# Kernel optimization log

Hardware: AMD Instinct MI355X
Metric: run time of the kernel (lower is better)

## Reference

```python
import jax, jax.numpy as jnp
import numpy as np

HID = 256   # hidden_dim
P = 16      # pool_size
EPS = 1e-5


def _ln(x, g, b):
    m = x.mean(-1, keepdims=True)
    v = x.var(-1, keepdims=True)
    return (x - m) * jax.lax.rsqrt(v + EPS) * g + b


def setup_inputs() -> dict:
    key = jax.random.key(0)
    ks = jax.random.split(key, 12)
    B, Cf, H, W = 8, 512, 64, 64
    Cg = Cf // 2
    Co = Cf // 2
    s = 0.02
    d = {}
    d['e_f'] = jax.random.normal(ks[0], (B, Cf, H, W), jnp.float32)
    d['e_g'] = jax.random.normal(ks[1], (B, Cg, H, W), jnp.float32)
    d['l_feat'] = jax.random.normal(ks[2], (B, 768, 20), jnp.float32)
    d['l_mask'] = jnp.ones((B, 20, 1), jnp.float32)
    d['ln_f_g'] = jnp.ones((Cf,), jnp.float32)
    d['ln_f_b'] = jnp.zeros((Cf,), jnp.float32)
    d['ln_g_g'] = jnp.ones((Cg,), jnp.float32)
    d['ln_g_b'] = jnp.zeros((Cg,), jnp.float32)
    d['wq'] = jax.random.normal(ks[3], (Cf, HID), jnp.float32) * s
    d['bq'] = jnp.zeros((HID,), jnp.float32)
    d['wk'] = jax.random.normal(ks[4], (Cg, HID), jnp.float32) * s
    d['bk'] = jnp.zeros((HID,), jnp.float32)
    d['wv'] = jax.random.normal(ks[5], (Cg, HID), jnp.float32) * s
    d['bv'] = jnp.zeros((HID,), jnp.float32)
    d['wo'] = jax.random.normal(ks[6], (HID, HID), jnp.float32) * s
    d['bo'] = jnp.zeros((HID,), jnp.float32)
    d['dw_k'] = jax.random.normal(ks[7], (HID, 1, 3, 3), jnp.float32) * s  # depthwise kernel (OIHW, I=1)
    d['efp_w'] = jax.random.normal(ks[8], (HID, Cf), jnp.float32) * s     # 1x1 conv v_channels->hidden
    d['efp_b'] = jnp.zeros((HID,), jnp.float32)
    d['outc_w'] = jax.random.normal(ks[9], (Co, HID), jnp.float32) * s    # 1x1 conv hidden->out
    d['outc_b'] = jnp.zeros((Co,), jnp.float32)
    d['bn_g'] = jnp.ones((Co,), jnp.float32)
    d['bn_b'] = jnp.zeros((Co,), jnp.float32)
    d['bn_m'] = jnp.zeros((Co,), jnp.float32)
    d['bn_v'] = jnp.ones((Co,), jnp.float32)
    return d


def reference(e_f, e_g, l_feat, l_mask, ln_f_g, ln_f_b, ln_g_g, ln_g_b,
              wq, bq, wk, bk, wv, bv, wo, bo, dw_k, efp_w, efp_b,
              outc_w, outc_b, bn_g, bn_b, bn_m, bn_v):
    B, Cf, H, W = e_f.shape
    # Q = w_qi(LN(e_f))                                  (B, HW, HID)
    q = _ln(e_f.transpose(0, 2, 3, 1), ln_f_g, ln_f_b).reshape(B, H * W, Cf) @ wq + bq
    # K/V projections from LN(e_g)
    g = _ln(e_g.transpose(0, 2, 3, 1), ln_g_g, ln_g_b).reshape(B, H * W, -1)
    k = (g @ wk + bk).reshape(B, H, W, HID)
    v = (g @ wv + bv).reshape(B, H, W, HID)
    # 16x16 max/avg pooling -> (B, Hp*Wp, HID)
    k = jnp.max(k.reshape(B, H // P, P, W // P, P, HID), axis=(2, 4)).reshape(B, -1, HID)
    v = jnp.mean(v.reshape(B, H // P, P, W // P, P, HID), axis=(2, 4)).reshape(B, -1, HID)
    # pooled attention
    attn = jax.nn.softmax(jnp.einsum('bqd,bkd->bqk', q, k) * (HID ** -0.5), axis=-1)
    a_i = jnp.einsum('bqk,bkd->bqd', attn, v)  # (B, HW, HID)
    # depthwise 3x3 conv on Q (NCHW)
    q_nchw = q.reshape(B, H, W, HID).transpose(0, 3, 1, 2)
    dw = jax.lax.conv_general_dilated(q_nchw, dw_k, (1, 1), [(1, 1), (1, 1)],
                                      feature_group_count=HID)
    combined = dw + a_i.reshape(B, H, W, HID).transpose(0, 3, 1, 2)
    comb = combined.transpose(0, 2, 3, 1).reshape(B, H * W, HID) @ wo + bo
    comb = comb.reshape(B, H, W, HID).transpose(0, 3, 1, 2)
    # 1x1 proj of e_f, elementwise gate
    efp = jnp.einsum('bchw,oc->bohw', e_f, efp_w) + efp_b[None, :, None, None]
    e_a = efp * comb
    # out: 1x1 conv + BN (inference) + ReLU (dropout inactive in eval)
    out = jnp.einsum('bchw,oc->bohw', e_a, outc_w) + outc_b[None, :, None, None]
    scale = (bn_g * jax.lax.rsqrt(bn_v + EPS))[None, :, None, None]
    out = (out - bn_m[None, :, None, None]) * scale + bn_b[None, :, None, None]
    return jax.nn.relu(out)
```

## Files before the change

### kernel.cpp

```cpp
#include <hip/hip_runtime.h>
#include <math.h>

#define EPS 1e-5f

typedef __attribute__((ext_vector_type(8))) short bf16x8;
typedef __attribute__((ext_vector_type(4))) float f32x4;

__device__ __forceinline__ unsigned short f2bf(float f) {
    unsigned int u = __float_as_uint(f);
    u += 0x7fff + ((u >> 16) & 1);
    return (unsigned short)(u >> 16);
}
__device__ __forceinline__ float bf2f(unsigned short h) {
    return __uint_as_float(((unsigned int)h) << 16);
}
__device__ __forceinline__ float lof(unsigned int u) {
    return __uint_as_float(u << 16);
}
__device__ __forceinline__ float hif(unsigned int u) {
    return __uint_as_float(u & 0xffff0000u);
}
__device__ __forceinline__ void async16(void* lds, const void* g) {
    __builtin_amdgcn_global_load_lds(
        (const __attribute__((address_space(1))) unsigned int*)g,
        (__attribute__((address_space(3))) unsigned int*)lds, 16, 0, 0);
}

__global__ __launch_bounds__(256) void trans_prep(
    const float* __restrict__ ef, const float* __restrict__ eg,
    unsigned short* __restrict__ ef_bf, unsigned short* __restrict__ eg_bf,
    float* __restrict__ pf, float* __restrict__ pfq,
    float* __restrict__ pg, float* __restrict__ pgq,
    const float* __restrict__ lnfg, const float* __restrict__ lnfb,
    const float* __restrict__ wq, const float* __restrict__ bq,
    const float* __restrict__ efpw, const float* __restrict__ efpb,
    const float* __restrict__ lngg, const float* __restrict__ lngb,
    const float* __restrict__ wk, const float* __restrict__ bk,
    const float* __restrict__ wv, const float* __restrict__ bv,
    const float* __restrict__ wo, const float* __restrict__ outcw,
    const float* __restrict__ outcb, const float* __restrict__ bng,
    const float* __restrict__ bnb, const float* __restrict__ bnm,
    const float* __restrict__ bnv, const float* __restrict__ dwk,
    unsigned short* __restrict__ Wb1t, unsigned short* __restrict__ Wb2t,
    unsigned short* __restrict__ Wot, unsigned short* __restrict__ Woc,
    float* __restrict__ dwt,
    float* __restrict__ cs1, float* __restrict__ cst1,
    float* __restrict__ cs2, float* __restrict__ cst2,
    float* __restrict__ scv, float* __restrict__ shv)
{
    __shared__ float tile[64][65];
    __shared__ float psum[4][64], pss[4][64];
    int id = blockIdx.x;
    int t = threadIdx.x;
    if (id < 3072) {
        const float* src; unsigned short* dst; float* ps; float* pq;
        int C, cblk, b, p0;
        if (id < 2048) {
            src = ef; dst = ef_bf; ps = pf; pq = pfq; C = 512;
            b = id >> 8; cblk = (id >> 5) & 7; p0 = (id & 31) * 128;
        } else {
            id -= 2048;
            src = eg; dst = eg_bf; ps = pg; pq = pgq; C = 256;
            b = id >> 7; cblk = (id >> 5) & 3; p0 = (id & 31) * 128;
        }
        int c0 = cblk * 64;
        const float* s = src + ((size_t)b * C + c0) * 4096 + p0;
        int cr = t >> 4, p4 = (t & 15) * 4;
        int lane = t & 63, grp = t >> 6;
        int pr = t >> 3, c8 = (t & 7) * 8;

        float4 r1[4], r2[4];
#pragma unroll
        for (int i = 0; i < 4; i++)
            r1[i] = *(const float4*)(s + (size_t)(i * 16 + cr) * 4096 + p4);
#pragma unroll
        for (int i = 0; i < 4; i++)
            r2[i] = *(const float4*)(s + (size_t)(i * 16 + cr) * 4096 + 64 + p4);

#pragma unroll
        for (int half = 0; half < 2; half++) {
#pragma unroll
            for (int i = 0; i < 4; i++) {
                float4 v = half ? r2[i] : r1[i];
                int c = i * 16 + cr;
                tile[c][p4 + 0] = v.x; tile[c][p4 + 1] = v.y;
                tile[c][p4 + 2] = v.z; tile[c][p4 + 3] = v.w;
            }
            __syncthreads();

            int pbase = p0 + half * 64;
            unsigned short* d = dst + ((size_t)(b * 4096 + pbase)) * C + c0;
#pragma unroll
            for (int i = 0; i < 2; i++) {
                int p = i * 32 + pr;
                uint4 pk;
                pk.x = (unsigned)f2bf(tile[c8 + 0][p]) | ((unsigned)f2bf(tile[c8 + 1][p]) << 16);
                pk.y = (unsigned)f2bf(tile[c8 + 2][p]) | ((unsigned)f2bf(tile[c8 + 3][p]) << 16);
                pk.z = (unsigned)f2bf(tile[c8 + 4][p]) | ((unsigned)f2bf(tile[c8 + 5][p]) << 16);
                pk.w = (unsigned)f2bf(tile[c8 + 6][p]) | ((unsigned)f2bf(tile[c8 + 7][p]) << 16);
                *(uint4*)(d + (size_t)p * C + c8) = pk;
            }

            float sm = 0.f, sq = 0.f;
#pragma unroll
            for (int j = 0; j < 16; j++) {
                float v = tile[grp * 16 + j][lane];
                sm += v; sq += v * v;
            }
            psum[grp][lane] = sm; pss[grp][lane] = sq;
            __syncthreads();
            if (t < 64) {
                float fs = psum[0][t] + psum[1][t] + psum[2][t] + psum[3][t];
                float fq = pss[0][t] + pss[1][t] + pss[2][t] + pss[3][t];
                ps[cblk * 32768 + b * 4096 + pbase + t] = fs;
                pq[cblk * 32768 + b * 4096 + pbase + t] = fq;
            }
            if (half == 0) __syncthreads();
        }
    } else {
        int id2 = id - 3072;
        float* red1 = (float*)psum;
        float* red2 = (float*)pss;
        if (id2 < 64) {
            const float* src; unsigned short* dst; const float* scale;
            int K, k0, n0;
            if (id2 < 32) {
                src = wq; dst = Wb1t; scale = lnfg; K = 512;
                k0 = (id2 >> 2) * 64; n0 = (id2 & 3) * 64;
            } else if (id2 < 48) {
                int j = id2 - 32;
                src = wk; dst = Wb2t; scale = lngg; K = 256;
                k0 = (j >> 2) * 64; n0 = (j & 3) * 64;
            } else {
                int j = id2 - 48;
                src = wo; dst = Wot; scale = nullptr; K = 256;
                k0 = (j >> 2) * 64; n0 = (j & 3) * 64;
            }
            int rr = t >> 6, cc = t & 63;
#pragma unroll
            for (int i = 0; i < 16; i++) {
                int r = i * 4 + rr;
                tile[r][cc] = src[(size_t)(k0 + r) * 256 + n0 + cc];
            }
            __syncthreads();
            int nn = t >> 3, k8 = (t & 7) * 8;
#pragma unroll
            for (int i = 0; i < 2; i++) {
                int n = i * 32 + nn;
                float v[8];
#pragma unroll
                for (int j = 0; j < 8; j++) {
                    float s = scale ? scale[k0 + k8 + j] : 1.f;
                    v[j] = s * tile[k8 + j][n];
                }
                uint4 pk;
                pk.x = (unsigned)f2bf(v[0]) | ((unsigned)f2bf(v[1]) << 16);
                pk.y = (unsigned)f2bf(v[2]) | ((unsigned)f2bf(v[3]) << 16);
                pk.z = (unsigned)f2bf(v[4]) | ((unsigned)f2bf(v[5]) << 16);
                pk.w = (unsigned)f2bf(v[6]) | ((unsigned)f2bf(v[7]) << 16);
                *(uint4*)(dst + (size_t)(n0 + n) * K + k0 + k8) = pk;
            }
        } else if (id2 < 192) {
            int j = (id2 - 64) * 1024 + t * 4;
            float4 v = *(const float4*)(efpw + j);
            uint2 pk;
            pk.x = (unsigned)f2bf(v.x) | ((unsigned)f2bf(v.y) << 16);
            pk.y = (unsigned)f2bf(v.z) | ((unsigned)f2bf(v.w) << 16);
            *(uint2*)(Wb1t + 131072 + j) = pk;
        } else if (id2 < 256) {
            int j = (id2 - 192) * 1024 + t * 4;
            float4 v = *(const float4*)(outcw + j);
            uint2 pk;
            pk.x = (unsigned)f2bf(v.x) | ((unsigned)f2bf(v.y) << 16);
            pk.y = (unsigned)f2bf(v.z) | ((unsigned)f2bf(v.w) << 16);
            *(uint2*)(Woc + j) = pk;
        } else if (id2 == 256) {
#pragma unroll
            for (int tap = 0; tap < 9; tap++)
                dwt[tap * 256 + t] = dwk[t * 9 + tap];
        } else if (id2 < 265) {
            int n0 = (id2 - 257) * 32;
            int nl = t & 31, kq = t >> 5;
            float cs = 0.f, ct = 0.f;
#pragma unroll 4
            for (int kk = 0; kk < 64; kk++) {
                int k = kq * 64 + kk;
                float w = wq[k * 256 + n0 + nl];
                cs += lnfg[k] * w; ct += lnfb[k] * w;
            }
            red1[kq * 32 + nl] = cs; red2[kq * 32 + nl] = ct;
            __syncthreads();
            if (t < 32) {
                float s = 0.f, c2 = 0.f;
#pragma unroll
                for (int q = 0; q < 8; q++) { s += red1[q * 32 + t]; c2 += red2[q * 32 + t]; }
                int n = n0 + t;
                cs1[n] = s; cst1[n] = c2 + bq[n];
                cs1[256 + n] = 0.f; cst1[256 + n] = efpb[n];
            }
        } else if (id2 < 273) {
            int n0 = (id2 - 265) * 32;
            int nl = t & 31, kq = t >> 5;
            float cs = 0.f, ct = 0.f;
#pragma unroll 4
            for (int kk = 0; kk < 32; kk++) {
                int k = kq * 32 + kk;
                float w = wk[k * 256 + n0 + nl];
                cs += lngg[k] * w; ct += lngb[k] * w;
            }
            red1[kq * 32 + nl] = cs; red2[kq * 32 + nl] = ct;
            __syncthreads();
            if (t < 32) {
                float s = 0.f, c2 = 0.f;
#pragma unroll
                for (int q = 0; q < 8; q++) { s += red1[q * 32 + t]; c2 += red2[q * 32 + t]; }
                int n = n0 + t;
                cs2[n] = s; cst2[n] = c2 + bk[n];
            }
        } else if (id2 < 281) {
            int n0 = (id2 - 273) * 32;
            int nl = t & 31, kq = t >> 5;
            float cs = 0.f, ct = 0.f;
#pragma unroll 4
            for (int kk = 0; kk < 32; kk++) {
                int k = kq * 32 + kk;
                float w = wv[k * 256 + n0 + nl];
                cs += lngg[k] * w; ct += lngb[k] * w;
            }
            red1[kq * 32 + nl] = cs; red2[kq * 32 + nl] = ct;
            __syncthreads();
            if (t < 32) {
                float s = 0.f, c2 = 0.f;
#pragma unroll
                for (int q = 0; q < 8; q++) { s += red1[q * 32 + t]; c2 += red2[q * 32 + t]; }
                int n = n0 + t;
                cs2[256 + n] = s; cst2[256 + n] = c2 + bv[n];
            }
        } else {
            int n = t;
            float s = bng[n] * rsqrtf(bnv[n] + EPS);
            scv[n] = s;
            shv[n] = (outcb[n] - bnm[n]) * s + bnb[n];
        }
    }
}

template<int K>
__device__ __forceinline__ void mfma_core(
    const unsigned short* __restrict__ A, const unsigned short* __restrict__ Bt,
    int m0, int n0, unsigned short* As, unsigned short* Bs, f32x4 acc[4][4])
{
    const int tid = threadIdx.x;
    const int wave = tid >> 6, lane = tid & 63;
    const int wm = (wave & 1) * 64, wn = (wave >> 1) * 64;
#pragma unroll
    for (int i = 0; i < 4; i++)
#pragma unroll
        for (int j = 0; j < 4; j++) acc[i][j] = (f32x4){0.f, 0.f, 0.f, 0.f};

    const int srow = wave * 32 + (lane >> 3);
    const int sg = (lane & 7) ^ ((lane >> 3) & 7);
    const unsigned short* ga = A + (size_t)(m0 + srow) * K + sg * 8;
    const unsigned short* gb = Bt + (size_t)(n0 + srow) * K + sg * 8;

    for (int k0 = 0; k0 < K; k0 += 64) {
#pragma unroll
        for (int t = 0; t < 4; t++) {
            async16(As + (wave * 32 + t * 8) * 64, ga + (size_t)t * 8 * K + k0);
            async16(Bs + (wave * 32 + t * 8) * 64, gb + (size_t)t * 8 * K + k0);
        }
        __syncthreads();
#pragma unroll
        for (int ks = 0; ks < 2; ks++) {
            bf16x8 af[4], bfr[4];
            int kb = ks * 4 + (lane >> 4);
            int slot = (kb ^ (lane & 7)) * 8;
#pragma unroll
            for (int i = 0; i < 4; i++) {
                int m = wm + i * 16 + (lane & 15);
                af[i] = *(const bf16x8*)&As[m * 64 + slot];
                int n = wn + i * 16 + (lane & 15);
                bfr[i] = *(const bf16x8*)&Bs[n * 64 + slot];
            }
#pragma unroll
            for (int i = 0; i < 4; i++)
#pragma unroll
                for (int j = 0; j < 4; j++)
                    acc[i][j] = __builtin_amdgcn_mfma_f32_16x16x32_bf16(
                        af[i], bfr[j], acc[i][j], 0, 0, 0);
        }
        __syncthreads();
    }
}

__global__ __launch_bounds__(256, 2) void gemm_proj(
    const unsigned short* __restrict__ ef_bf, const unsigned short* __restrict__ Wb1t,
    const float* __restrict__ cs1, const float* __restrict__ cst1,
    const float* __restrict__ pf, const float* __restrict__ pfq,
    unsigned short* __restrict__ qbuf, unsigned short* __restrict__ efpbuf,
    const unsigned short* __restrict__ eg_bf, const unsigned short* __restrict__ Wb2t,
    const float* __restrict__ cs2, const float* __restrict__ cst2,
    const float* __restrict__ pg, const float* __restrict__ pgq,
    unsigned short* __restrict__ kfull,
    const float* __restrict__ eg, float* __restrict__ s1,
    float* __restrict__ s0)
{
    __shared__ unsigned short As[128 * 64];
    __shared__ unsigned short Bs[256 * 64];
    __shared__ float sstat[256];
    const int tid = threadIdx.x;
    const int wave = tid >> 6, lane = tid & 63;
    const int bid = blockIdx.x;

    if (bid < 512) {
        float* smem = (float*)Bs;
        const int id3 = bid;
        int b = id3 >> 6, hp = (id3 >> 4) & 3, cgrp = id3 & 15;
        int rr = tid >> 4, cq = tid & 15;
        int p = (hp * 16 + rr) * 64 + cq * 4;

        float w[4], m[4];
#pragma unroll
        for (int d = 0; d < 4; d++) {
            int gp = b * 4096 + p + d;
            float s = 0.f, q = 0.f;
#pragma unroll
            for (int i = 0; i < 4; i++) { s += pg[i * 32768 + gp]; q += pgq[i * 32768 + gp]; }
            float mean = s * (1.f / 256.f);
            m[d] = mean;
            w[d] = rsqrtf(q * (1.f / 256.f) - mean * mean + EPS);
        }

        float part[16];
        const float* egb = eg + ((size_t)b * 256 + cgrp * 16) * 4096 + p;
#pragma unroll
        for (int cc = 0; cc < 16; cc++) {
            float4 v4 = *(const float4*)(egb + (size_t)cc * 4096);
            part[cc] = w[0] * v4.x + w[1] * v4.y + w[2] * v4.z + w[3] * v4.w;
        }
#pragma unroll
        for (int cc = 0; cc < 16; cc++) smem[tid * 16 + cc] = part[cc];
        if (cgrp == 0)
            smem[4096 + tid] = w[0] * m[0] + w[1] * m[1] + w[2] * m[2] + w[3] * m[3];
        __syncthreads();
        if (tid < 64) {
            int cx2 = tid >> 4, cc = tid & 15;
            float sacc = 0.f;
#pragma unroll
            for (int rr2 = 0; rr2 < 16; rr2++)
#pragma unroll
                for (int dq = 0; dq < 4; dq++)
                    sacc += smem[(rr2 * 16 + cx2 * 4 + dq) * 16 + cc];
            s1[((size_t)(b * 16 + hp * 4 + cx2)) * 256 + cgrp * 16 + cc] = sacc;
        }
        if (cgrp == 0 && tid < 4) {
            float sacc = 0.f;
#pragma unroll
            for (int rr2 = 0; rr2 < 16; rr2++)
#pragma unroll
                for (int dq = 0; dq < 4; dq++)
                    sacc += smem[4096 + rr2 * 16 + tid * 4 + dq];
            s0[b * 16 + hp * 4 + tid] = sacc;
        }
    } else if (bid < 1024) {
        const int bid1 = bid - 512;
        const int m0 = (bid1 >> 1) * 128, n0 = (bid1 & 1) * 256;
        const int wm = (wave & 1) * 64, wn = (wave >> 1) * 128;
        f32x4 acc[4][8];

        if (tid < 128) {
            int gm = m0 + tid;
            float s = 0.f, q = 0.f;
#pragma unroll
            for (int i = 0; i < 8; i++) { s += pf[i * 32768 + gm]; q += pfq[i * 32768 + gm]; }
            float m = s * (1.f / 512.f);
            sstat[tid] = m;
            sstat[128 + tid] = rsqrtf(q * (1.f / 512.f) - m * m + EPS);
        }

#pragma unroll
        for (int i = 0; i < 4; i++)
#pragma unroll
            for (int j = 0; j < 8; j++) acc[i][j] = (f32x4){0.f, 0.f, 0.f, 0.f};

        const int srow = lane >> 3;
        const int sg = (lane & 7) ^ (srow & 7);
        const unsigned short* ga = ef_bf + (size_t)(m0 + wave * 32 + srow) * 512 + sg * 8;
        const unsigned short* gb = Wb1t + (size_t)(n0 + wave * 64 + srow) * 512 + sg * 8;

        for (int k0 = 0; k0 < 512; k0 += 64) {
#pragma unroll
            for (int t = 0; t < 4; t++)
                async16(As + (wave * 32 + t * 8) * 64, ga + (size_t)t * 8 * 512 + k0);
#pragma unroll
            for (int t = 0; t < 8; t++)
                async16(Bs + (wave * 64 + t * 8) * 64, gb + (size_t)t * 8 * 512 + k0);
            __syncthreads();
#pragma unroll
            for (int ks = 0; ks < 2; ks++) {
                bf16x8 af[4], bfr[8];
                int kb = ks * 4 + (lane >> 4);
                int slot = (kb ^ (lane & 7)) * 8;
#pragma unroll
                for (int i = 0; i < 4; i++)
                    af[i] = *(const bf16x8*)&As[(wm + i * 16 + (lane & 15)) * 64 + slot];
#pragma unroll
                for (int j = 0; j < 8; j++)
                    bfr[j] = *(const bf16x8*)&Bs[(wn + j * 16 + (lane & 15)) * 64 + slot];
#pragma unroll
                for (int i = 0; i < 4; i++)
#pragma unroll
                    for (int j = 0; j < 8; j++)
                        acc[i][j] = __builtin_amdgcn_mfma_f32_16x16x32_bf16(
                            af[i], bfr[j], acc[i][j], 0, 0, 0);
            }
            __syncthreads();
        }

        bool isq = (n0 == 0);
#pragma unroll
        for (int i = 0; i < 4; i++) {
#pragma unroll
            for (int r = 0; r < 4; r++) {
                int lm = wm + i * 16 + ((lane >> 4) * 4) + r;
                int gm = m0 + lm;
                float mean = sstat[lm], rs = sstat[128 + lm];
#pragma unroll
                for (int j = 0; j < 8; j++) {
                    int nn = wn + j * 16 + (lane & 15);
                    float v = acc[i][j][r];
                    if (isq) {
                        int n = nn;
                        float o = rs * (v - mean * cs1[n]) + cst1[n];
                        qbuf[(size_t)gm * 256 + nn] = f2bf(o);
                    } else {
                        int n = nn + 256;
                        efpbuf[(size_t)gm * 256 + nn] = f2bf(v + cst1[n]);
                    }
                }
            }
        }
    } else {
        const int j2 = bid - 1024;
        const int m0 = (j2 >> 1) * 128, n0 = (j2 & 1) * 128;
        f32x4 acc[4][4];

        if (tid < 128) {
            int gm = m0 + tid;
            float s = 0.f, q = 0.f;
#pragma unroll
            for (int i = 0; i < 4; i++) { s += pg[i * 32768 + gm]; q += pgq[i * 32768 + gm]; }
            float m = s * (1.f / 256.f);
            float r = rsqrtf(q * (1.f / 256.f) - m * m + EPS);
            sstat[tid] = m; sstat[128 + tid] = r;
        }

        mfma_core<256>(eg_bf, Wb2t, m0, n0, As, Bs, acc);
        int wm = (wave & 1) * 64, wn = (wave >> 1) * 64;
#pragma unroll
        for (int i = 0; i < 4; i++) {
#pragma unroll
            for (int r = 0; r < 4; r++) {
                int lm = wm + i * 16 + ((lane >> 4) * 4) + r;
                int gm = m0 + lm;
                float mean = sstat[lm], rs = sstat[128 + lm];
#pragma unroll
                for (int j = 0; j < 4; j++) {
                    int n = n0 + wn + j * 16 + (lane & 15);
                    float o = rs * (acc[i][j][r] - mean * cs2[n]) + cst2[n];
                    kfull[(size_t)gm * 256 + n] = f2bf(o);
                }
            }
        }
    }
}

__global__ __launch_bounds__(256) void pool_vp(
    const unsigned short* __restrict__ kfull, unsigned short* __restrict__ kpb,
    const float* __restrict__ s1, const float* __restrict__ s0,
    const float* __restrict__ lngg, const float* __restrict__ wv,
    const float* __restrict__ cs2, const float* __restrict__ cst2,
    float* __restrict__ vp)
{
    __shared__ float smem[2048];
    int id = blockIdx.x;
    int t = threadIdx.x;
    if (id < 128) {
        int b = id >> 4, cell = id & 15;
        int hp = cell >> 2, wp = cell & 3;
        int g8 = t & 31, rr = t >> 5;
        float kmx[8];
#pragma unroll
        for (int j = 0; j < 8; j++) kmx[j] = -3.402823466e38f;
#pragma unroll
        for (int rsub = 0; rsub < 2; rsub++) {
            int r = rr * 2 + rsub;
            int prow = (hp * 16 + r) * 64 + wp * 16;
            for (int cl = 0; cl < 16; cl++) {
                size_t basei = ((size_t)(b * 4096 + prow + cl)) * 256 + g8 * 8;
                uint4 kv = *(const uint4*)(kfull + basei);
                kmx[0] = fmaxf(kmx[0], lof(kv.x)); kmx[1] = fmaxf(kmx[1], hif(kv.x));
                kmx[2] = fmaxf(kmx[2], lof(kv.y)); kmx[3] = fmaxf(kmx[3], hif(kv.y));
                kmx[4] = fmaxf(kmx[4], lof(kv.z)); kmx[5] = fmaxf(kmx[5], hif(kv.z));
                kmx[6] = fmaxf(kmx[6], lof(kv.w)); kmx[7] = fmaxf(kmx[7], hif(kv.w));
            }
        }
#pragma unroll
        for (int j = 0; j < 8; j++) smem[rr * 256 + g8 * 8 + j] = kmx[j];
        __syncthreads();
        float m = smem[t];
#pragma unroll
        for (int r2 = 1; r2 < 8; r2++) m = fmaxf(m, smem[r2 * 256 + t]);
        kpb[(size_t)(b * 16 + cell) * 256 + t] = f2bf(m);
    } else {
        int cell = id - 128;
        int n = t;
        const float* s1r = s1 + (size_t)cell * 256;
        float acc = 0.f;
        for (int c = 0; c < 256; c++)
            acc = fmaf(lngg[c] * s1r[c], wv[c * 256 + n], acc);
        vp[(size_t)cell * 256 + n] = acc * (1.f / 256.f)
            - (s0[cell] * (1.f / 256.f)) * cs2[256 + n] + cst2[256 + n];
    }
}

__global__ __launch_bounds__(256) void combined_dw(
    const unsigned short* __restrict__ qbuf, const unsigned short* __restrict__ kpb,
    const float* __restrict__ vp, const float* __restrict__ dwt,
    unsigned short* __restrict__ combined)
{
    __shared__ float attns[1024];
    int wave = threadIdx.x >> 6, lane = threadIdx.x & 63;
    int id = blockIdx.x;
    int b = id & 7, row = id >> 3;
    int pidx0 = row * 64 + wave * 16;
    int h = row;

    {
        int fr = lane & 15, quad = lane >> 4;
        const unsigned short* qrow =
            qbuf + (size_t)(b * 4096 + pidx0 + fr) * 256 + quad * 8;
        const unsigned short* krow = kpb + (size_t)(b * 16 + fr) * 256 + quad * 8;
        f32x4 sacc = {0.f, 0.f, 0.f, 0.f};
#pragma unroll
        for (int ks = 0; ks < 8; ks++) {
            bf16x8 af = *(const bf16x8*)(qrow + ks * 32);
            bf16x8 bf_ = *(const bf16x8*)(krow + ks * 32);
            sacc = __builtin_amdgcn_mfma_f32_16x16x32_bf16(af, bf_, sacc, 0, 0, 0);
        }
#pragma unroll
        for (int r = 0; r < 4; r++) {
            float s = sacc[r] * 0.0625f;
            float mx = s;
#pragma unroll
            for (int off = 8; off >= 1; off >>= 1) mx = fmaxf(mx, __shfl_xor(mx, off));
            float e = __expf(s - mx);
            float sum = e;
#pragma unroll
            for (int off = 8; off >= 1; off >>= 1) sum += __shfl_xor(sum, off);
            attns[wave * 256 + (quad * 4 + r) * 16 + fr] = e / sum;
        }
    }
    __syncthreads();

    int o4 = lane * 4;
    float4 kreg[9];
#pragma unroll
    for (int tap = 0; tap < 9; tap++)
        kreg[tap] = *(const float4*)&dwt[tap * 256 + o4];
    const float* arow_base = attns + wave * 256;

#pragma unroll
    for (int sub = 0; sub < 4; sub++) {
        int pidx = pidx0 + sub * 4;
        int w0 = pidx & 63;
        float4 acc[4];
#pragma unroll
        for (int i = 0; i < 4; i++) acc[i] = (float4){0.f, 0.f, 0.f, 0.f};
#pragma unroll
        for (int c = 0; c < 16; c++) {
            float4 v = *(const float4*)&vp[(size_t)(b * 16 + c) * 256 + o4];
#pragma unroll
            for (int i = 0; i < 4; i++) {
                float a = arow_base[(sub * 4 + i) * 16 + c];
                acc[i].x = fmaf(a, v.x, acc[i].x); acc[i].y = fmaf(a, v.y, acc[i].y);
                acc[i].z = fmaf(a, v.z, acc[i].z); acc[i].w = fmaf(a, v.w, acc[i].w);
            }
        }
#pragma unroll
        for (int dy = 0; dy < 3; dy++) {
            int hh = h + dy - 1;
            if (hh < 0 || hh > 63) continue;
            const unsigned short* qr = qbuf + ((size_t)(b * 4096 + hh * 64)) * 256;
            float4 ft[6];
#pragma unroll
            for (int c = 0; c < 6; c++) {
                int xx = w0 - 1 + c;
                if (xx < 0 || xx > 63) {
                    ft[c] = (float4){0.f, 0.f, 0.f, 0.f};
                } else {
                    uint2 qa = *(const uint2*)(qr + (size_t)xx * 256 + o4);
                    ft[c] = (float4){lof(qa.x), hif(qa.x), lof(qa.y), hif(qa.y)};
                }
            }
#pragma unroll
            for (int dx = 0; dx < 3; dx++) {
                float4 kk = kreg[dy * 3 + dx];
#pragma unroll
                for (int i = 0; i < 4; i++) {
                    float4 qv = ft[i + dx];
                    acc[i].x = fmaf(qv.x, kk.x, acc[i].x);
                    acc[i].y = fmaf(qv.y, kk.y, acc[i].y);
                    acc[i].z = fmaf(qv.z, kk.z, acc[i].z);
                    acc[i].w = fmaf(qv.w, kk.w, acc[i].w);
                }
            }
        }
#pragma unroll
        for (int i = 0; i < 4; i++) {
            uint2 pk;
            pk.x = (unsigned)f2bf(acc[i].x) | ((unsigned)f2bf(acc[i].y) << 16);
            pk.y = (unsigned)f2bf(acc[i].z) | ((unsigned)f2bf(acc[i].w) << 16);
            *(uint2*)(combined + ((size_t)(b * 4096 + pidx + i)) * 256 + o4) = pk;
        }
    }
}

__global__ __launch_bounds__(256) void gemm34_mfma(
    const unsigned short* __restrict__ comb, const unsigned short* __restrict__ Wot,
    const float* __restrict__ bo, const unsigned short* __restrict__ efp,
    const unsigned short* __restrict__ Woc,
    const float* __restrict__ scv, const float* __restrict__ shv,
    float* __restrict__ outp)
{
    __shared__ unsigned short As[64 * 64];
    __shared__ unsigned short Bs[256 * 64];
    __shared__ unsigned short eat[64 * 256];
    const int tid = threadIdx.x;
    const int wave = tid >> 6, lane = tid & 63;
    const int m0 = blockIdx.x * 64;

    const int srow = lane >> 3;
    const int sg = (lane & 7) ^ (srow & 7);

    f32x4 acc[4][4];
#pragma unroll
    for (int i = 0; i < 4; i++)
#pragma unroll
        for (int j = 0; j < 4; j++) acc[i][j] = (f32x4){0.f, 0.f, 0.f, 0.f};

    const unsigned short* ga = comb + (size_t)(m0 + wave * 16 + srow) * 256 + sg * 8;
    const unsigned short* gb = Wot + (size_t)(wave * 64 + srow) * 256 + sg * 8;

    for (int k0 = 0; k0 < 256; k0 += 64) {
#pragma unroll
        for (int t = 0; t < 2; t++)
            async16(As + (wave * 16 + t * 8) * 64, ga + (size_t)t * 8 * 256 + k0);
#pragma unroll
        for (int t = 0; t < 8; t++)
            async16(Bs + (wave * 64 + t * 8) * 64, gb + (size_t)t * 8 * 256 + k0);
        __syncthreads();
#pragma unroll
        for (int ks = 0; ks < 2; ks++) {
            bf16x8 af[4], bfr[4];
            int kb = ks * 4 + (lane >> 4);
            int slot = (kb ^ (lane & 7)) * 8;
#pragma unroll
            for (int i = 0; i < 4; i++) {
                af[i]  = *(const bf16x8*)&As[(i * 16 + (lane & 15)) * 64 + slot];
                bfr[i] = *(const bf16x8*)&Bs[(wave * 64 + i * 16 + (lane & 15)) * 64 + slot];
            }
#pragma unroll
            for (int i = 0; i < 4; i++)
#pragma unroll
                for (int j = 0; j < 4; j++)
                    acc[i][j] = __builtin_amdgcn_mfma_f32_16x16x32_bf16(
                        af[i], bfr[j], acc[i][j], 0, 0, 0);
        }
        __syncthreads();
    }

    float bo4[4];
#pragma unroll
    for (int j = 0; j < 4; j++) bo4[j] = bo[wave * 64 + j * 16 + (lane & 15)];
#pragma unroll
    for (int i = 0; i < 4; i++) {
#pragma unroll
        for (int r = 0; r < 4; r++) {
            int pos = i * 16 + ((lane >> 4) * 4) + r;
#pragma unroll
            for (int j = 0; j < 4; j++) {
                int n = wave * 64 + j * 16 + (lane & 15);
                float o = (acc[i][j][r] + bo4[j])
                          * bf2f(efp[(size_t)(m0 + pos) * 256 + n]);
                int o8 = j * 2 + ((lane >> 3) & 1);
                int slot = o8 ^ (pos & 7);
                eat[pos * 256 + wave * 64 + slot * 8 + (lane & 7)] = f2bf(o);
            }
        }
    }

    f32x4 acc2[4][4];
#pragma unroll
    for (int i = 0; i < 4; i++)
#pragma unroll
        for (int j = 0; j < 4; j++) acc2[i][j] = (f32x4){0.f, 0.f, 0.f, 0.f};

    const unsigned short* gw = Woc + (size_t)(wave * 64 + srow) * 256 + sg * 8;
    for (int k0 = 0; k0 < 256; k0 += 64) {
#pragma unroll
        for (int t = 0; t < 8; t++)
            async16(Bs + (wave * 64 + t * 8) * 64, gw + (size_t)t * 8 * 256 + k0);
        __syncthreads();
        int kc = k0 >> 6;
#pragma unroll
        for (int ks = 0; ks < 2; ks++) {
            bf16x8 af2[4], bf2_[4];
            int kb = ks * 4 + (lane >> 4);
            int slot = (kb ^ (lane & 7)) * 8;
#pragma unroll
            for (int i = 0; i < 4; i++) {
                af2[i]  = *(const bf16x8*)&Bs[(wave * 64 + i * 16 + (lane & 15)) * 64 + slot];
                bf2_[i] = *(const bf16x8*)&eat[(i * 16 + (lane & 15)) * 256 + kc * 64 + slot];
            }
#pragma unroll
            for (int i = 0; i < 4; i++)
#pragma unroll
                for (int j = 0; j < 4; j++)
                    acc2[i][j] = __builtin_amdgcn_mfma_f32_16x16x32_bf16(
                        af2[i], bf2_[j], acc2[i][j], 0, 0, 0);
        }
        __syncthreads();
    }

#pragma unroll
    for (int i = 0; i < 4; i++) {
#pragma unroll
        for (int r = 0; r < 4; r++) {
            int co = wave * 64 + i * 16 + ((lane >> 4) * 4) + r;
            float s = scv[co], hh = shv[co];
#pragma unroll
            for (int j = 0; j < 4; j++) {
                int p = m0 + j * 16 + (lane & 15);
                float o = fmaxf(fmaf(acc2[i][j][r], s, hh), 0.f);
                outp[((size_t)(p >> 12)) * 1048576 + (size_t)co * 4096 + (p & 4095)] = o;
            }
        }
    }
}

extern "C" void kernel_launch(void* const* d_in, const int* in_sizes, int n_in,
                              void* d_out, int out_size, void* d_ws, size_t ws_size,
                              hipStream_t stream)
{
    const float* e_f   = (const float*)d_in[0];
    const float* e_g   = (const float*)d_in[1];
    const float* lnfg  = (const float*)d_in[4];
    const float* lnfb  = (const float*)d_in[5];
    const float* lngg  = (const float*)d_in[6];
    const float* lngb  = (const float*)d_in[7];
    const float* wq    = (const float*)d_in[8];
    const float* bq    = (const float*)d_in[9];
    const float* wk    = (const float*)d_in[10];
    const float* bk    = (const float*)d_in[11];
    const float* wv    = (const float*)d_in[12];
    const float* bv    = (const float*)d_in[13];
    const float* wo    = (const float*)d_in[14];
    const float* bo    = (const float*)d_in[15];
    const float* dwk   = (const float*)d_in[16];
    const float* efpw  = (const float*)d_in[17];
    const float* efpb  = (const float*)d_in[18];
    const float* outcw = (const float*)d_in[19];
    const float* outcb = (const float*)d_in[20];
    const float* bng   = (const float*)d_in[21];
    const float* bnb   = (const float*)d_in[22];
    const float* bnm   = (const float*)d_in[23];
    const float* bnv   = (const float*)d_in[24];
    float* outp = (float*)d_out;

    char* base = (char*)d_ws;
    auto alloc = [&](size_t bytes) -> char* {
        char* r = base; base += (bytes + 255) & ~(size_t)255; return r;
    };
    float* pf    = (float*)alloc(8 * 32768 * 4);
    float* pfq   = (float*)alloc(8 * 32768 * 4);
    float* pg    = (float*)alloc(4 * 32768 * 4);
    float* pgq   = (float*)alloc(4 * 32768 * 4);
    float* cs1   = (float*)alloc(512 * 4);
    float* cst1  = (float*)alloc(512 * 4);
    float* cs2   = (float*)alloc(512 * 4);
    float* cst2  = (float*)alloc(512 * 4);
    float* scv   = (float*)alloc(256 * 4);
    float* shv   = (float*)alloc(256 * 4);
    float* dwt   = (float*)alloc(9 * 256 * 4);
    unsigned short* Wb1t = (unsigned short*)alloc(262144 * 2);
    unsigned short* Wb2t = (unsigned short*)alloc(65536 * 2);
    unsigned short* Wot  = (unsigned short*)alloc(65536 * 2);
    unsigned short* Woc  = (unsigned short*)alloc(65536 * 2);
    unsigned short* ef_bf = (unsigned short*)alloc((size_t)32768 * 512 * 2);
    unsigned short* eg_bf = (unsigned short*)alloc((size_t)32768 * 256 * 2);
    unsigned short* qbuf  = (unsigned short*)alloc((size_t)32768 * 256 * 2);
    unsigned short* efpbuf = (unsigned short*)alloc((size_t)32768 * 256 * 2);
    unsigned short* kfull = (unsigned short*)alloc((size_t)32768 * 256 * 2);
    unsigned short* kpb  = (unsigned short*)alloc(128 * 256 * 2);
    float* vp    = (float*)alloc(128 * 256 * 4);
    float* s1    = (float*)alloc(128 * 256 * 4);
    float* s0    = (float*)alloc(128 * 4);

    trans_prep<<<3354, 256, 0, stream>>>(
        e_f, e_g, ef_bf, eg_bf, pf, pfq, pg, pgq,
        lnfg, lnfb, wq, bq, efpw, efpb, lngg, lngb, wk, bk, wv, bv, wo,
        outcw, outcb, bng, bnb, bnm, bnv, dwk,
        Wb1t, Wb2t, Wot, Woc, dwt, cs1, cst1, cs2, cst2, scv, shv);
    gemm_proj<<<1536, 256, 0, stream>>>(
        ef_bf, Wb1t, cs1, cst1, pf, pfq, qbuf, efpbuf,
        eg_bf, Wb2t, cs2, cst2, pg, pgq, kfull,
        e_g, s1, s0);
    pool_vp<<<256, 256, 0, stream>>>(kfull, kpb, s1, s0, lngg, wv, cs2, cst2, vp);
    combined_dw<<<512, 256, 0, stream>>>(qbuf, kpb, vp, dwt, kfull);
    gemm34_mfma<<<512, 256, 0, stream>>>(kfull, Wot, bo, efpbuf,
                                         Woc, scv, shv, outp);
}
```

Before: 287.5 us.

## Double-buffer LDS tiles in projection GEMMs to overlap loads with MFMA

Both GEMM paths in gemm_proj now keep two LDS buffers with a K-step of 32 instead of one buffer with a K-step of 64. The next tile is prefetched asynchronously while MFMAs run on the current one, leaving one barrier per step instead of two. The LDS swizzle is rewritten for the narrower 32-wide rows. The aim is to hide global-load latency behind compute, at the cost of twice as many loop iterations and a changed bank-conflict pattern.

```diff
diff --git a/kernel.cpp b/kernel.cpp
--- a/kernel.cpp
+++ b/kernel.cpp
@@ -245,54 +245,6 @@
     }
 }
 
-template<int K>
-__device__ __forceinline__ void mfma_core(
-    const unsigned short* __restrict__ A, const unsigned short* __restrict__ Bt,
-    int m0, int n0, unsigned short* As, unsigned short* Bs, f32x4 acc[4][4])
-{
-    const int tid = threadIdx.x;
-    const int wave = tid >> 6, lane = tid & 63;
-    const int wm = (wave & 1) * 64, wn = (wave >> 1) * 64;
-#pragma unroll
-    for (int i = 0; i < 4; i++)
-#pragma unroll
-        for (int j = 0; j < 4; j++) acc[i][j] = (f32x4){0.f, 0.f, 0.f, 0.f};
-
-    const int srow = wave * 32 + (lane >> 3);
-    const int sg = (lane & 7) ^ ((lane >> 3) & 7);
-    const unsigned short* ga = A + (size_t)(m0 + srow) * K + sg * 8;
-    const unsigned short* gb = Bt + (size_t)(n0 + srow) * K + sg * 8;
-
-    for (int k0 = 0; k0 < K; k0 += 64) {
-#pragma unroll
-        for (int t = 0; t < 4; t++) {
-            async16(As + (wave * 32 + t * 8) * 64, ga + (size_t)t * 8 * K + k0);
-            async16(Bs + (wave * 32 + t * 8) * 64, gb + (size_t)t * 8 * K + k0);
-        }
-        __syncthreads();
-#pragma unroll
-        for (int ks = 0; ks < 2; ks++) {
-            bf16x8 af[4], bfr[4];
-            int kb = ks * 4 + (lane >> 4);
-            int slot = (kb ^ (lane & 7)) * 8;
-#pragma unroll
-            for (int i = 0; i < 4; i++) {
-                int m = wm + i * 16 + (lane & 15);
-                af[i] = *(const bf16x8*)&As[m * 64 + slot];
-                int n = wn + i * 16 + (lane & 15);
-                bfr[i] = *(const bf16x8*)&Bs[n * 64 + slot];
-            }
-#pragma unroll
-            for (int i = 0; i < 4; i++)
-#pragma unroll
-                for (int j = 0; j < 4; j++)
-                    acc[i][j] = __builtin_amdgcn_mfma_f32_16x16x32_bf16(
-                        af[i], bfr[j], acc[i][j], 0, 0, 0);
-        }
-        __syncthreads();
-    }
-}
-
 __global__ __launch_bounds__(256, 2) void gemm_proj(
     const unsigned short* __restrict__ ef_bf, const unsigned short* __restrict__ Wb1t,
     const float* __restrict__ cs1, const float* __restrict__ cst1,
@@ -305,12 +257,16 @@
     const float* __restrict__ eg, float* __restrict__ s1,
     float* __restrict__ s0)
 {
-    __shared__ unsigned short As[128 * 64];
-    __shared__ unsigned short Bs[256 * 64];
+    __shared__ unsigned short As[2][128 * 32];
+    __shared__ unsigned short Bs[2][256 * 32];
     __shared__ float sstat[256];
     const int tid = threadIdx.x;
     const int wave = tid >> 6, lane = tid & 63;
     const int bid = blockIdx.x;
+
+    const int slr = lane >> 2;
+    const int soc = (lane & 3) ^ ((lane >> 3) & 3);
+    const int slot = ((lane >> 4) ^ (((lane & 15) >> 1) & 3)) * 8;
 
     if (bid < 512) {
         float* smem = (float*)Bs;
@@ -383,38 +339,45 @@
 #pragma unroll
             for (int j = 0; j < 8; j++) acc[i][j] = (f32x4){0.f, 0.f, 0.f, 0.f};
 
-        const int srow = lane >> 3;
-        const int sg = (lane & 7) ^ (srow & 7);
-        const unsigned short* ga = ef_bf + (size_t)(m0 + wave * 32 + srow) * 512 + sg * 8;
-        const unsigned short* gb = Wb1t + (size_t)(n0 + wave * 64 + srow) * 512 + sg * 8;
-
-        for (int k0 = 0; k0 < 512; k0 += 64) {
-#pragma unroll
-            for (int t = 0; t < 4; t++)
-                async16(As + (wave * 32 + t * 8) * 64, ga + (size_t)t * 8 * 512 + k0);
-#pragma unroll
-            for (int t = 0; t < 8; t++)
-                async16(Bs + (wave * 64 + t * 8) * 64, gb + (size_t)t * 8 * 512 + k0);
+        const unsigned short* ga = ef_bf + (size_t)(m0 + wave * 32 + slr) * 512 + soc * 8;
+        const unsigned short* gb = Wb1t + (size_t)(n0 + wave * 64 + slr) * 512 + soc * 8;
+
+#pragma unroll
+        for (int tt = 0; tt < 2; tt++)
+            async16(&As[0][(wave * 32 + tt * 16) * 32], ga + (size_t)tt * 16 * 512);
+#pragma unroll
+        for (int tt = 0; tt < 4; tt++)
+            async16(&Bs[0][(wave * 64 + tt * 16) * 32], gb + (size_t)tt * 16 * 512);
+        __syncthreads();
+
+        int cur = 0;
+        for (int s = 0; s < 16; s++) {
+            if (s < 15) {
+                int kk = (s + 1) * 32;
+#pragma unroll
+                for (int tt = 0; tt < 2; tt++)
+                    async16(&As[cur ^ 1][(wave * 32 + tt * 16) * 32],
+                            ga + (size_t)tt * 16 * 512 + kk);
+#pragma unroll
+                for (int tt = 0; tt < 4; tt++)
+                    async16(&Bs[cur ^ 1][(wave * 64 + tt * 16) * 32],
+                            gb + (size_t)tt * 16 * 512 + kk);
+            }
+            bf16x8 af[4], bfr[8];
+#pragma unroll
+            for (int i = 0; i < 4; i++)
+                af[i] = *(const bf16x8*)&As[cur][(wm + i * 16 + (lane & 15)) * 32 + slot];
+#pragma unroll
+            for (int j = 0; j < 8; j++)
+                bfr[j] = *(const bf16x8*)&Bs[cur][(wn + j * 16 + (lane & 15)) * 32 + slot];
+#pragma unroll
+            for (int i = 0; i < 4; i++)
+#pragma unroll
+                for (int j = 0; j < 8; j++)
+                    acc[i][j] = __builtin_amdgcn_mfma_f32_16x16x32_bf16(
+                        af[i], bfr[j], acc[i][j], 0, 0, 0);
             __syncthreads();
-#pragma unroll
-            for (int ks = 0; ks < 2; ks++) {
-                bf16x8 af[4], bfr[8];
-                int kb = ks * 4 + (lane >> 4);
-                int slot = (kb ^ (lane & 7)) * 8;
-#pragma unroll
-                for (int i = 0; i < 4; i++)
-                    af[i] = *(const bf16x8*)&As[(wm + i * 16 + (lane & 15)) * 64 + slot];
-#pragma unroll
-                for (int j = 0; j < 8; j++)
-                    bfr[j] = *(const bf16x8*)&Bs[(wn + j * 16 + (lane & 15)) * 64 + slot];
-#pragma unroll
-                for (int i = 0; i < 4; i++)
-#pragma unroll
-                    for (int j = 0; j < 8; j++)
-                        acc[i][j] = __builtin_amdgcn_mfma_f32_16x16x32_bf16(
-                            af[i], bfr[j], acc[i][j], 0, 0, 0);
-            }
-            __syncthreads();
+            cur ^= 1;
         }
 
         bool isq = (n0 == 0);
@@ -443,6 +406,7 @@
     } else {
         const int j2 = bid - 1024;
         const int m0 = (j2 >> 1) * 128, n0 = (j2 & 1) * 128;
+        const int wm = (wave & 1) * 64, wn = (wave >> 1) * 64;
         f32x4 acc[4][4];
 
         if (tid < 128) {
@@ -455,8 +419,49 @@
             sstat[tid] = m; sstat[128 + tid] = r;
         }
 
-        mfma_core<256>(eg_bf, Wb2t, m0, n0, As, Bs, acc);
-        int wm = (wave & 1) * 64, wn = (wave >> 1) * 64;
+#pragma unroll
+        for (int i = 0; i < 4; i++)
+#pragma unroll
+            for (int j = 0; j < 4; j++) acc[i][j] = (f32x4){0.f, 0.f, 0.f, 0.f};
+
+        const unsigned short* ga = eg_bf + (size_t)(m0 + wave * 32 + slr) * 256 + soc * 8;
+        const unsigned short* gb = Wb2t + (size_t)(n0 + wave * 32 + slr) * 256 + soc * 8;
+
+#pragma unroll
+        for (int tt = 0; tt < 2; tt++) {
+            async16(&As[0][(wave * 32 + tt * 16) * 32], ga + (size_t)tt * 16 * 256);
+            async16(&Bs[0][(wave * 32 + tt * 16) * 32], gb + (size_t)tt * 16 * 256);
+        }
+        __syncthreads();
+
+        int cur = 0;
+        for (int s = 0; s < 8; s++) {
+            if (s < 7) {
+                int kk = (s + 1) * 32;
+#pragma unroll
+                for (int tt = 0; tt < 2; tt++) {
+                    async16(&As[cur ^ 1][(wave * 32 + tt * 16) * 32],
+                            ga + (size_t)tt * 16 * 256 + kk);
+                    async16(&Bs[cur ^ 1][(wave * 32 + tt * 16) * 32],
+                            gb + (size_t)tt * 16 * 256 + kk);
+                }
+            }
+            bf16x8 af[4], bfr[4];
+#pragma unroll
+            for (int i = 0; i < 4; i++) {
+                af[i]  = *(const bf16x8*)&As[cur][(wm + i * 16 + (lane & 15)) * 32 + slot];
+                bfr[i] = *(const bf16x8*)&Bs[cur][(wn + i * 16 + (lane & 15)) * 32 + slot];
+            }
+#pragma unroll
+            for (int i = 0; i < 4; i++)
+#pragma unroll
+                for (int j = 0; j < 4; j++)
+                    acc[i][j] = __builtin_amdgcn_mfma_f32_16x16x32_bf16(
+                        af[i], bfr[j], acc[i][j], 0, 0, 0);
+            __syncthreads();
+            cur ^= 1;
+        }
+
 #pragma unroll
         for (int i = 0; i < 4; i++) {
 #pragma unroll
```

New measurement: 289.2 us. No clear change (+0.6%).
